# Kernel tuning notes

Measured on AMD Instinct MI355X. Metric: run time of the kernel, lower is better.

Reference implementation:

```python
import jax, jax.numpy as jnp
import numpy as np

B, S, D = 8, 1024, 512
H, DH, OUT = 8, 64, 512
EPS = 1e-6

def _ln(x, scale, bias):
    m = jnp.mean(x, -1, keepdims=True)
    v = jnp.mean(jnp.square(x - m), -1, keepdims=True)
    return (x - m) * jax.lax.rsqrt(v + EPS) * scale + bias

def _rel_shift(x):
    # TransformerXL relative shift: [B,H,Q,P] -> [B,H,Q,P]
    b, h, q, p = x.shape
    x = jnp.pad(x, ((0, 0), (0, 0), (0, 0), (1, 0)))
    x = x.reshape(b, h, p + 1, q)
    return x[:, :, 1:, :].reshape(b, h, q, p)

def _gate(x, y, wry, wrx, wzy, wzx, why, whx, bg):
    # GTrXL GRU-style gating
    r = jax.nn.sigmoid(y @ wry + x @ wrx)
    z = jax.nn.sigmoid(y @ wzy + x @ wzx - bg)
    h = jnp.tanh(y @ why + (r * x) @ whx)
    return (1 - z) * x + z * h

def setup_inputs() -> dict:
    key = jax.random.key(0)
    ks = jax.random.split(key, 40)
    w = lambda k, shp: (0.02 * jax.random.normal(k, shp, jnp.float32))
    inp = {
        'values_keys': jax.random.normal(ks[0], (B, S, D), jnp.float32),
        'queries': jax.random.normal(ks[1], (B, S, D), jnp.float32),
        'pos_embed': jax.random.normal(ks[2], (S, D), jnp.float32),
        'mask': jnp.tril(jnp.ones((S, S), bool))[None, None],
        'ln1_scale': jnp.ones((D,), jnp.float32), 'ln1_bias': jnp.zeros((D,), jnp.float32),
        'wq': w(ks[3], (D, H, DH)), 'bq': jnp.zeros((H, DH), jnp.float32),
        'wk': w(ks[4], (D, H, DH)), 'bk': jnp.zeros((H, DH), jnp.float32),
        'wv': w(ks[5], (D, H, DH)), 'bv': jnp.zeros((H, DH), jnp.float32),
        'wr': w(ks[6], (D, H, DH)),
        'u_bias': w(ks[7], (H, DH)), 'v_bias': w(ks[8], (H, DH)),
        'wo': w(ks[9], (H, DH, OUT)), 'bo': jnp.zeros((OUT,), jnp.float32),
        'ln2_scale': jnp.ones((OUT,), jnp.float32), 'ln2_bias': jnp.zeros((OUT,), jnp.float32),
        'w1': w(ks[10], (OUT, OUT)), 'b1': jnp.zeros((OUT,), jnp.float32),
        'w2': w(ks[11], (OUT, OUT)), 'b2': jnp.zeros((OUT,), jnp.float32),
    }
    for gi, base in ((1, 12), (2, 19)):
        for j, nm in enumerate(['wry', 'wrx', 'wzy', 'wzx', 'why', 'whx']):
            inp['g%d_%s' % (gi, nm)] = w(ks[base + j], (OUT, OUT))
        inp['g%d_bg' % gi] = 2.0 * jnp.ones((OUT,), jnp.float32)
    return inp

def reference(values_keys, queries, pos_embed, mask, ln1_scale, ln1_bias, wq, bq, wk, bk, wv, bv, wr, u_bias, v_bias, wo, bo, ln2_scale, ln2_bias, w1, b1, w2, b2, g1_wry, g1_wrx, g1_wzy, g1_wzx, g1_why, g1_whx, g1_bg, g2_wry, g2_wrx, g2_wzy, g2_wzx, g2_why, g2_whx, g2_bg):
    vk = _ln(values_keys, ln1_scale, ln1_bias)
    qn = _ln(queries, ln1_scale, ln1_bias)
    q = jnp.einsum('bsd,dhk->bshk', qn, wq) + bq
    k = jnp.einsum('bsd,dhk->bshk', vk, wk) + bk
    v = jnp.einsum('bsd,dhk->bshk', vk, wv) + bv
    r = jnp.einsum('pd,dhk->phk', pos_embed, wr)
    ac = jnp.einsum('bqhk,bshk->bhqs', q + u_bias, k)
    bd = _rel_shift(jnp.einsum('bqhk,phk->bhqp', q + v_bias, r))
    scores = (ac + bd) * jnp.float32(1.0 / np.sqrt(DH))
    scores = jnp.where(mask, scores, jnp.float32(-1e9))
    attn = jax.nn.softmax(scores, axis=-1)
    o = jnp.einsum('bhqs,bshk->bqhk', attn, v)
    attn_out = jnp.einsum('bqhk,hko->bqo', o, wo) + bo
    out_attention = _gate(queries, jax.nn.relu(attn_out), g1_wry, g1_wrx, g1_wzy, g1_wzx, g1_why, g1_whx, g1_bg)
    h = _ln(out_attention, ln2_scale, ln2_bias)
    h = jax.nn.gelu(h @ w1 + b1) @ w2 + b2
    return _gate(h, jax.nn.relu(out_attention), g2_wry, g2_wrx, g2_wzy, g2_wzx, g2_why, g2_whx, g2_bg)
```

## Files before the change

kernel.cpp:

```cpp
#include <hip/hip_runtime.h>
#include <hip/hip_bf16.h>
#include <math.h>

#define TPB 256
#define B_   8
#define S_   1024
#define D_   512
#define H_   8
#define DH_  64
#define MTOK (B_ * S_)
#define NEL  (MTOK * D_)
#define WMAT (D_ * D_)

typedef __attribute__((ext_vector_type(8))) short bf8;
typedef __attribute__((ext_vector_type(4))) float f4;

__device__ __forceinline__ float ld_any(const void* p, long i, bool bf) {
  if (bf) {
    unsigned u = (unsigned)((const unsigned short*)p)[i];
    union { unsigned u; float f; } c; c.u = u << 16;
    return c.f;
  }
  return ((const float*)p)[i];
}

__device__ __forceinline__ unsigned short f2bf(float f) {
  union { float f; unsigned u; } c; c.f = f;
  unsigned u = c.u;
  u += 0x7FFFu + ((u >> 16) & 1u);
  return (unsigned short)(u >> 16);
}

typedef const void __attribute__((address_space(1)))* gp_t;
typedef void __attribute__((address_space(3)))* lp_t;
__device__ __forceinline__ void gl16(const void* g, void* l) {
  __builtin_amdgcn_global_load_lds((gp_t)(uintptr_t)g,
                                   (lp_t)(unsigned)(uintptr_t)l, 16, 0, 0);
}

struct P19 { const void* p[19]; };
struct P14 { const void* p[14]; };

__device__ __forceinline__ void ln_row(const void* src, unsigned short* dst,
                                       long row, const void* scale,
                                       const void* bias, bool bf_s, bool bf_p,
                                       int t, float* red) {
  long base = row * 512;
  float a = ld_any(src, base + t, bf_s), b = ld_any(src, base + t + 256, bf_s);
  red[t] = a + b;
  __syncthreads();
  for (int s = 128; s > 0; s >>= 1) { if (t < s) red[t] += red[t + s]; __syncthreads(); }
  float m = red[0] * (1.0f / 512.0f);
  __syncthreads();
  float da = a - m, db = b - m;
  red[t] = da * da + db * db;
  __syncthreads();
  for (int s = 128; s > 0; s >>= 1) { if (t < s) red[t] += red[t + s]; __syncthreads(); }
  float inv = rsqrtf(red[0] * (1.0f / 512.0f) + 1e-6f);
  dst[base + t] = f2bf(da * inv * ld_any(scale, t, bf_p) + ld_any(bias, t, bf_p));
  dst[base + t + 256] =
      f2bf(db * inv * ld_any(scale, t + 256, bf_p) + ld_any(bias, t + 256, bf_p));
}

__global__ __launch_bounds__(TPB) void k_prep(
    const void* __restrict__ vk_src, const void* __restrict__ q_src,
    const void* __restrict__ pos_src, const void* __restrict__ sc_src,
    const void* __restrict__ bi_src, P19 pw, P14 pp,
    unsigned short* __restrict__ vk_b, unsigned short* __restrict__ qn_b,
    float* __restrict__ qF, unsigned short* __restrict__ qB,
    unsigned short* __restrict__ posB, float* __restrict__ Pb,
    unsigned short* __restrict__ Wt, const unsigned* __restrict__ flagp) {
  __shared__ float smem[64 * 65];
  const bool bf = (*flagp == 0x3F803F80u);
  const int bx = blockIdx.x, t = threadIdx.x;
  if (bx < 16384) {
    long row = bx;
    const void* src = vk_src; unsigned short* dst = vk_b;
    if (row >= MTOK) { src = q_src; dst = qn_b; row -= MTOK; }
    ln_row(src, dst, row, sc_src, bi_src, bf, bf, t, smem);
  } else if (bx < 34844) {
    int bid = bx - 16384;
    if (bid < 16384) {
      long i = (long)bid * TPB + t;
      float v = ld_any(q_src, i, bf);
      qF[i] = v; qB[i] = f2bf(v);
    } else if (bid < 18432) {
      long i = (long)(bid - 16384) * TPB + t;
      posB[i] = f2bf(ld_any(pos_src, i, bf));
    } else {
      int i = (bid - 18432) * TPB + t;
      Pb[i] = ld_any(pp.p[i >> 9], i & 511, bf);
    }
  } else {
    int zz = bx - 34844;
    int z = zz >> 6, tile = zz & 63;
    int k0 = (tile >> 3) * 64, n0 = (tile & 7) * 64;
    const void* src = pw.p[z];
    unsigned short* dst = Wt + (size_t)z * WMAT;
#pragma unroll
    for (int i = 0; i < 16; i++) {
      int fl = i * TPB + t;
      int r = fl >> 6, c = fl & 63;
      smem[r * 65 + c] = ld_any(src, (long)(k0 + r) * 512 + n0 + c, bf);
    }
    __syncthreads();
#pragma unroll
    for (int i = 0; i < 16; i++) {
      int fl = i * TPB + t;
      int r = fl >> 6, c = fl & 63;
      dst[(size_t)(n0 + r) * 512 + k0 + c] = f2bf(smem[c * 65 + r]);
    }
  }
}

__global__ __launch_bounds__(TPB) void k_ln_bf(const void* __restrict__ src,
                                               unsigned short* __restrict__ dst,
                                               const float* __restrict__ scale,
                                               const float* __restrict__ bias) {
  __shared__ float red[TPB];
  ln_row(src, dst, blockIdx.x, scale, bias, false, false, threadIdx.x, red);
}

__device__ __forceinline__ void gemm_core(
    unsigned short* As, unsigned short* Bs,
    const unsigned short* __restrict__ A1, const unsigned short* __restrict__ W1,
    const unsigned short* __restrict__ A2, const unsigned short* __restrict__ W2,
    const float* __restrict__ bias, const float* __restrict__ xb,
    const float* __restrict__ zb, const float* __restrict__ aux1,
    const float* __restrict__ aux2,
    float* __restrict__ outF, unsigned short* __restrict__ outB,
    unsigned short* __restrict__ outB2,
    const unsigned* __restrict__ flagp, int ACT, int bm, int bn) {
  const int tid = threadIdx.x;
  const int w = tid >> 6, lane = tid & 63;
  const int quad = lane >> 4, col = lane & 15;
  const int lrow = lane >> 3;
  const int lkc  = (lane & 7) ^ lrow;
  const int sw_base = col & 7;

  f4 acc[2][2];
#pragma unroll
  for (int mi = 0; mi < 2; mi++)
#pragma unroll
    for (int ni = 0; ni < 2; ni++) acc[mi][ni] = (f4){0.f, 0.f, 0.f, 0.f};

  for (int prod = 0; prod < 2; ++prod) {
    const unsigned short* Ap = prod ? A2 : A1;
    const unsigned short* Wp = prod ? W2 : W1;
    if (!Ap) break;
    for (int k0 = 0; k0 < 512; k0 += 64) {
      __syncthreads();
      gl16(Ap + (size_t)(bm + w * 8 + lrow) * 512 + k0 + lkc * 8,
           (char*)As + w * 1024);
      const unsigned short* bS = Wp + (size_t)(bn + w * 8 + lrow) * 512 + k0 + lkc * 8;
      gl16(bS,                    (char*)Bs + w * 1024);
      gl16(bS + (size_t)32 * 512, (char*)Bs + 4096 + w * 1024);
      gl16(bS + (size_t)64 * 512, (char*)Bs + 8192 + w * 1024);
      gl16(bS + (size_t)96 * 512, (char*)Bs + 12288 + w * 1024);
      __syncthreads();
#pragma unroll
      for (int kk = 0; kk < 2; ++kk) {
        const int swz = (kk * 4 + quad) ^ sw_base;
        bf8 af[2], bfg[2];
#pragma unroll
        for (int mi = 0; mi < 2; mi++)
          af[mi] = *(const bf8*)&As[((mi * 16 + col) * 8 + swz) * 8];
#pragma unroll
        for (int ni = 0; ni < 2; ni++)
          bfg[ni] = *(const bf8*)&Bs[((w * 32 + ni * 16 + col) * 8 + swz) * 8];
#pragma unroll
        for (int mi = 0; mi < 2; mi++)
#pragma unroll
          for (int ni = 0; ni < 2; ni++)
            acc[mi][ni] = __builtin_amdgcn_mfma_f32_16x16x32_bf16(af[mi], bfg[ni],
                                                                  acc[mi][ni], 0, 0, 0);
      }
    }
  }

  const bool bfout = flagp && (*flagp == 0x3F803F80u);
#pragma unroll
  for (int mi = 0; mi < 2; mi++)
#pragma unroll
    for (int ni = 0; ni < 2; ni++) {
      const int n = bn + w * 32 + ni * 16 + col;
      const float bn_v = bias ? bias[n] : 0.f;
      const int m0 = bm + mi * 16 + quad * 4;
      if (ACT == 11 && n >= 512) {
        unsigned long long pk = 0;
#pragma unroll
        for (int r = 0; r < 4; r++) {
          float v = acc[mi][ni][r] + bn_v;
          pk |= (unsigned long long)f2bf(v) << (16 * r);
        }
        size_t dst = ((size_t)(m0 >> 10) * 512 + (n - 512)) * 1024 + (m0 & 1023);
        *(unsigned long long*)&outB2[dst] = pk;
      } else {
#pragma unroll
        for (int r = 0; r < 4; r++) {
          size_t idx = (size_t)(m0 + r) * 512 + n;
          float v = acc[mi][ni][r] + bn_v;
          if (ACT == 0) {
            if (outF) outF[idx] = v;
            if (outB) outB[idx] = f2bf(v);
          } else if (ACT == 1) {
            outB[idx] = f2bf(fmaxf(v, 0.f));
          } else if (ACT == 5) {
            float z = zb[idx], x = xb[idx];
            float g = (1.f - z) * x + z * tanhf(v);
            outF[idx] = g;
            outB[idx] = f2bf(fmaxf(g, 0.f));
          } else if (ACT == 6) {
            float t = 0.7978845608028654f * (v + 0.044715f * v * v * v);
            outB[idx] = f2bf(0.5f * v * (1.f + tanhf(t)));
          } else if (ACT == 7) {
            float z = zb[idx], x = xb[idx];
            float g = (1.f - z) * x + z * tanhf(v);
            if (bfout) outB[idx] = f2bf(g);
            else       outF[idx] = g;
          } else if (ACT == 8) {
            outB[idx]  = f2bf(v + aux1[n]);
            outB2[idx] = f2bf(v + aux2[n]);
          } else if (ACT == 10) {
            if (n < 512) {
              outB[idx] = f2bf(xb[idx] / (1.f + __expf(-v)));
            } else {
              size_t zi = (size_t)(m0 + r) * 512 + (n - 512);
              outF[zi] = 1.f / (1.f + __expf(-(v - aux1[n - 512])));
            }
          } else if (ACT == 11) {
            outB[idx] = f2bf(v);
          }
        }
      }
    }
}

__global__ __launch_bounds__(TPB) void k_gemm(
    const unsigned short* __restrict__ A1, const unsigned short* __restrict__ W1,
    const unsigned short* __restrict__ A2, const unsigned short* __restrict__ W2,
    const float* __restrict__ bias, const float* __restrict__ xb,
    const float* __restrict__ zb, const float* __restrict__ aux1,
    const float* __restrict__ aux2,
    float* __restrict__ outF, unsigned short* __restrict__ outB,
    unsigned short* __restrict__ outB2,
    const unsigned* __restrict__ flagp, int ACT) {
  __shared__ unsigned short As[32 * 64];
  __shared__ unsigned short Bs[128 * 64];
  gemm_core(As, Bs, A1, W1, A2, W2, bias, xb, zb, aux1, aux2,
            outF, outB, outB2, flagp, ACT,
            blockIdx.x * 32, blockIdx.y * 128);
}

__global__ __launch_bounds__(TPB) void k_proj(
    const unsigned short* __restrict__ qn_b, const unsigned short* __restrict__ vk_b,
    const unsigned short* __restrict__ pos_b, const unsigned short* __restrict__ Wt,
    const float* __restrict__ Pb,
    unsigned short* __restrict__ qu_b, unsigned short* __restrict__ qv_b,
    unsigned short* __restrict__ k_b, unsigned short* __restrict__ vT,
    unsigned short* __restrict__ r_b) {
  __shared__ unsigned short As[32 * 64];
  __shared__ unsigned short Bs[128 * 64];
  const int bx = blockIdx.x;
  if (bx < 1024) {
    int bm = (bx & 255) * 32, bn = (bx >> 8) * 128;
    gemm_core(As, Bs, qn_b, Wt, nullptr, nullptr, Pb + 1024, nullptr, nullptr,
              Pb + 2560, Pb + 3072, nullptr, qu_b, qv_b, nullptr, 8, bm, bn);
  } else if (bx < 3072) {
    int t = bx - 1024;
    int bm = (t & 255) * 32, bn = (t >> 8) * 128;
    gemm_core(As, Bs, vk_b, Wt + (size_t)1 * WMAT, nullptr, nullptr, Pb + 1536,
              nullptr, nullptr, nullptr, nullptr, nullptr, k_b, vT, nullptr,
              11, bm, bn);
  } else {
    int t = bx - 3072;
    int bm = (t & 31) * 32, bn = (t >> 5) * 128;
    gemm_core(As, Bs, pos_b, Wt + (size_t)3 * WMAT, nullptr, nullptr, nullptr,
              nullptr, nullptr, nullptr, nullptr, nullptr, r_b, nullptr,
              nullptr, 0, bm, bn);
  }
}

#define AC_STR 68
#define BD_STR 100

__global__ __launch_bounds__(128) void k_attn3(
    const unsigned short* __restrict__ quB, const unsigned short* __restrict__ qvB,
    const unsigned short* __restrict__ kB, const unsigned short* __restrict__ vT,
    const unsigned short* __restrict__ rB, unsigned short* __restrict__ oB) {
  __shared__ float acS[2][16 * AC_STR];
  __shared__ float bdS[2][16 * BD_STR];
  const int tid = threadIdx.x;
  const int w = tid >> 6, lane = tid & 63;
  const int quad = lane >> 4, col = lane & 15;
  const int hh = w;
  const int bx = blockIdx.x;
  const int bh = (bx & 7) * 8 + ((bx >> 3) & 7);
  const int i  = bx >> 6;
  const int b = bh >> 3, h = bh & 7, dbase = h * 64;
  float* acw = acS[w];
  float* bdw = bdS[w];
  const float* acp = acS[w ^ 1];
  const float* bdp = bdS[w ^ 1];

  const int qts[2] = {63 - i, i};
#pragma unroll 1
  for (int ti = 0; ti < 2; ++ti) {
    const int qt = qts[ti];
    const int q0 = qt << 4;
    const int np = (qt >> 2) + 1;
    bf8 aqu[2], aqv[2];
    {
      const unsigned short* p1 = quB + (size_t)(b * 1024 + q0 + col) * 512 + dbase + quad * 8;
      const unsigned short* p2 = qvB + (size_t)(b * 1024 + q0 + col) * 512 + dbase + quad * 8;
      aqu[0] = *(const bf8*)p1; aqu[1] = *(const bf8*)(p1 + 32);
      aqv[0] = *(const bf8*)p2; aqv[1] = *(const bf8*)(p2 + 32);
    }
    f4 accO[4];
#pragma unroll
    for (int nd = 0; nd < 4; nd++) accO[nd] = (f4){0.f, 0.f, 0.f, 0.f};
    float lsum = 0.f;

#pragma unroll 1
    for (int pt = hh; pt < np; pt += 2) {
      const int p0 = pt << 6;
      const int j0 = 1008 - q0 + p0;
      f4 ac[4], bd[5];
#pragma unroll
      for (int ni = 0; ni < 4; ni++) ac[ni] = (f4){0.f, 0.f, 0.f, 0.f};
#pragma unroll
      for (int nj = 0; nj < 5; nj++) bd[nj] = (f4){0.f, 0.f, 0.f, 0.f};
#pragma unroll
      for (int ks = 0; ks < 2; ++ks) {
        const int dof = dbase + ks * 32 + quad * 8;
#pragma unroll
        for (int ni = 0; ni < 4; ++ni) {
          bf8 kb = *(const bf8*)&kB[(size_t)(b * 1024 + p0 + ni * 16 + col) * 512 + dof];
          ac[ni] = __builtin_amdgcn_mfma_f32_16x16x32_bf16(aqu[ks], kb, ac[ni], 0, 0, 0);
        }
#pragma unroll
        for (int nj = 0; nj < 5; ++nj) {
          int j = j0 + nj * 16 + col; if (j > 1023) j = 1023;
          bf8 rb = *(const bf8*)&rB[(size_t)j * 512 + dof];
          bd[nj] = __builtin_amdgcn_mfma_f32_16x16x32_bf16(aqv[ks], rb, bd[nj], 0, 0, 0);
        }
      }
#pragma unroll
      for (int ni = 0; ni < 4; ++ni)
#pragma unroll
        for (int r = 0; r < 4; ++r)
          acw[(quad * 4 + r) * AC_STR + ni * 16 + col] = ac[ni][r];
#pragma unroll
      for (int nj = 0; nj < 5; ++nj)
#pragma unroll
        for (int r = 0; r < 4; ++r) {
          int row = quad * 4 + r;
          bdw[row * BD_STR + 1 + nj * 16 + col + row] = bd[nj][r];
        }
      __asm__ volatile("s_waitcnt lgkmcnt(0)" ::: "memory");

      bf8 apf[2];
      const int qg = q0 + col;
#pragma unroll
      for (int ks = 0; ks < 2; ++ks) {
        const int po = ks * 32 + quad * 8;
        f4 A0 = *(const f4*)&acw[col * AC_STR + po];
        f4 A1 = *(const f4*)&acw[col * AC_STR + po + 4];
        f4 B0 = *(const f4*)&bdw[col * BD_STR + 16 + po];
        f4 B1 = *(const f4*)&bdw[col * BD_STR + 16 + po + 4];
        const int pb = p0 + po;
        union { bf8 v; unsigned short s[8]; } ap;
#pragma unroll
        for (int jj = 0; jj < 4; ++jj) {
          float e0 = (pb + jj <= qg) ? __expf((A0[jj] + B0[jj]) * 0.125f) : 0.f;
          float e1 = (pb + 4 + jj <= qg) ? __expf((A1[jj] + B1[jj]) * 0.125f) : 0.f;
          lsum += e0 + e1;
          ap.s[jj] = f2bf(e0); ap.s[4 + jj] = f2bf(e1);
        }
        apf[ks] = ap.v;
      }
#pragma unroll
      for (int ks = 0; ks < 2; ++ks) {
#pragma unroll
        for (int nd = 0; nd < 4; ++nd) {
          bf8 vb = *(const bf8*)&vT[(size_t)(bh * 64 + nd * 16 + col) * 1024 +
                                    p0 + ks * 32 + quad * 8];
          accO[nd] = __builtin_amdgcn_mfma_f32_16x16x32_bf16(apf[ks], vb, accO[nd], 0, 0, 0);
        }
      }
    }

#pragma unroll
    for (int nd = 0; nd < 4; ++nd)
#pragma unroll
      for (int r = 0; r < 4; ++r)
        acw[lane * 17 + nd * 4 + r] = accO[nd][r];
    bdw[lane] = lsum;
    __syncthreads();
    if (hh == 0) {
#pragma unroll
      for (int nd = 0; nd < 4; ++nd)
#pragma unroll
        for (int r = 0; r < 4; ++r)
          accO[nd][r] += acp[lane * 17 + nd * 4 + r];
      float ls = lsum + bdp[lane];
      ls += __shfl_xor(ls, 16, 64);
      ls += __shfl_xor(ls, 32, 64);
      float lr[4];
#pragma unroll
      for (int r = 0; r < 4; ++r) lr[r] = __shfl(ls, quad * 4 + r, 64);
#pragma unroll
      for (int nd = 0; nd < 4; ++nd)
#pragma unroll
        for (int r = 0; r < 4; ++r) {
          float o = accO[nd][r] / lr[r];
          oB[(size_t)(b * 1024 + q0 + quad * 4 + r) * 512 + dbase + nd * 16 + col] = f2bf(o);
        }
    }
    __syncthreads();
  }
}

extern "C" void kernel_launch(void* const* d_in, const int* in_sizes, int n_in,
                              void* d_out, int out_size, void* d_ws, size_t ws_size,
                              hipStream_t stream) {
  (void)in_sizes; (void)n_in; (void)out_size; (void)ws_size;
  const unsigned* flagp = (const unsigned*)d_in[4];
  char* ws = (char*)d_ws;
  const size_t MB = 1u << 20;
  auto SH = [&](int i) { return (unsigned short*)(ws + (size_t)i * 8 * MB); };

  unsigned short* vk_b = SH(0);
  unsigned short* qn_b = SH(1);
  unsigned short* qu_b = SH(2);
  unsigned short* qv_b = SH(3);
  unsigned short* k_b  = SH(4);
  unsigned short* qr_b = SH(5);
  unsigned short* vT   = SH(6);
  unsigned short* posr = SH(7);
  float* qF = (float*)(ws + 64 * MB);
  float* z1 = (float*)(ws + 80 * MB);
  float* oa = (float*)(ws + 96 * MB);
  unsigned short* Wt = (unsigned short*)(ws + 112 * MB);
  float* Pb = (float*)(ws + 122 * MB);

  unsigned short* pos_b = posr;
  unsigned short* r_b   = posr + 524288;
  unsigned short* o_b = qn_b;  unsigned short* y1 = vk_b;
  unsigned short* rx1 = qu_b;  unsigned short* y2 = qv_b;
  unsigned short* ln2h = k_b;  unsigned short* hg = qr_b;
  unsigned short* h_b = vT;    unsigned short* rx2 = posr;
  float* hF = qF;              float* z2 = z1;

  auto W = [&](int i) { return Wt + (size_t)i * WMAT; };
  dim3 bt(TPB);
  dim3 gG(MTOK / 32, 4);
  dim3 gG2(MTOK / 32, 8);

  P19 pw; const int wi[19] = {6, 8, 10, 12, 15, 19, 21,
                              23, 25, 24, 26, 27, 28, 30, 32, 31, 33, 34, 35};
  for (int i = 0; i < 19; i++) pw.p[i] = d_in[wi[i]];
  P14 pp; const int pi[14] = {4, 5, 7, 9, 11, 13, 14, 16, 17, 18, 20, 22, 29, 36};
  for (int i = 0; i < 14; i++) pp.p[i] = d_in[pi[i]];

  k_prep<<<dim3(36060), bt, 0, stream>>>(d_in[0], d_in[1], d_in[2], d_in[4],
                                         d_in[5], pw, pp, vk_b, qn_b, qF, qr_b,
                                         pos_b, Pb, Wt, flagp);

  k_proj<<<dim3(3200), bt, 0, stream>>>(qn_b, vk_b, pos_b, Wt, Pb,
                                        qu_b, qv_b, k_b, vT, r_b);

  k_attn3<<<dim3(2048), dim3(128), 0, stream>>>(qu_b, qv_b, k_b, vT, r_b, o_b);

  k_gemm<<<gG, bt, 0, stream>>>(o_b, W(4), nullptr, nullptr, Pb + 3584, nullptr,
                                nullptr, nullptr, nullptr, nullptr, y1, nullptr,
                                nullptr, 1);
  k_gemm<<<gG2, bt, 0, stream>>>(y1, W(7), qr_b, W(9), nullptr, qF, nullptr,
                                 Pb + 6144, nullptr, z1, rx1, nullptr,
                                 nullptr, 10);
  k_gemm<<<gG, bt, 0, stream>>>(y1, W(11), rx1, W(12), nullptr, qF, z1,
                                nullptr, nullptr, oa, y2, nullptr, nullptr, 5);

  k_ln_bf<<<dim3(MTOK), bt, 0, stream>>>(oa, ln2h, Pb + 4096, Pb + 4608);
  k_gemm<<<gG, bt, 0, stream>>>(ln2h, W(5), nullptr, nullptr, Pb + 5120, nullptr,
                                nullptr, nullptr, nullptr, nullptr, hg, nullptr,
                                nullptr, 6);
  k_gemm<<<gG, bt, 0, stream>>>(hg, W(6), nullptr, nullptr, Pb + 5632, nullptr,
                                nullptr, nullptr, nullptr, hF, h_b, nullptr,
                                nullptr, 0);

  k_gemm<<<gG2, bt, 0, stream>>>(y2, W(13), h_b, W(15), nullptr, hF, nullptr,
                                 Pb + 6656, nullptr, z2, rx2, nullptr,
                                 nullptr, 10);
  k_gemm<<<gG, bt, 0, stream>>>(y2, W(17), rx2, W(18), nullptr, hF, z2,
                                nullptr, nullptr, (float*)d_out,
                                (unsigned short*)d_out, nullptr, flagp, 7);
}
```

Measured before the change: 541.0 us.

## Use one wave per query tile in attention, dropping intra-block split and reduction

The attention kernel now launches 4096 single-wave blocks, each owning one 16-row query tile and walking all of its key tiles. Previously each 2-wave block handled a paired short and long query tile for load balance and split key tiles across waves, merging partial sums through shared memory with barriers. The new layout removes the cross-wave merge and syncs and shrinks the bd shared buffer with a bounds-checked shifted write. In exchange, blocks now vary widely in work (causal tiles from 1 to 16 key tiles), so load balance depends on the scheduler, and each wave's loop is serial.

```diff
diff --git a/kernel.cpp b/kernel.cpp
--- a/kernel.cpp
+++ b/kernel.cpp
@@ -282,143 +282,118 @@
 }
 
 #define AC_STR 68
-#define BD_STR 100
-
-__global__ __launch_bounds__(128) void k_attn3(
+#define BD_STR 68
+
+__global__ __launch_bounds__(64, 4) void k_attn4(
     const unsigned short* __restrict__ quB, const unsigned short* __restrict__ qvB,
     const unsigned short* __restrict__ kB, const unsigned short* __restrict__ vT,
     const unsigned short* __restrict__ rB, unsigned short* __restrict__ oB) {
-  __shared__ float acS[2][16 * AC_STR];
-  __shared__ float bdS[2][16 * BD_STR];
-  const int tid = threadIdx.x;
-  const int w = tid >> 6, lane = tid & 63;
+  __shared__ float acS[16 * AC_STR];
+  __shared__ float bdS[16 * BD_STR];
+  const int lane = threadIdx.x;
   const int quad = lane >> 4, col = lane & 15;
-  const int hh = w;
   const int bx = blockIdx.x;
   const int bh = (bx & 7) * 8 + ((bx >> 3) & 7);
-  const int i  = bx >> 6;
+  const int qt = 63 - (bx >> 6);
   const int b = bh >> 3, h = bh & 7, dbase = h * 64;
-  float* acw = acS[w];
-  float* bdw = bdS[w];
-  const float* acp = acS[w ^ 1];
-  const float* bdp = bdS[w ^ 1];
-
-  const int qts[2] = {63 - i, i};
+  const int q0 = qt << 4;
+  const int np = (qt >> 2) + 1;
+
+  bf8 aqu[2], aqv[2];
+  {
+    const unsigned short* p1 = quB + (size_t)(b * 1024 + q0 + col) * 512 + dbase + quad * 8;
+    const unsigned short* p2 = qvB + (size_t)(b * 1024 + q0 + col) * 512 + dbase + quad * 8;
+    aqu[0] = *(const bf8*)p1; aqu[1] = *(const bf8*)(p1 + 32);
+    aqv[0] = *(const bf8*)p2; aqv[1] = *(const bf8*)(p2 + 32);
+  }
+  f4 accO[4];
+#pragma unroll
+  for (int nd = 0; nd < 4; nd++) accO[nd] = (f4){0.f, 0.f, 0.f, 0.f};
+  float lsum = 0.f;
+
 #pragma unroll 1
-  for (int ti = 0; ti < 2; ++ti) {
-    const int qt = qts[ti];
-    const int q0 = qt << 4;
-    const int np = (qt >> 2) + 1;
-    bf8 aqu[2], aqv[2];
-    {
-      const unsigned short* p1 = quB + (size_t)(b * 1024 + q0 + col) * 512 + dbase + quad * 8;
-      const unsigned short* p2 = qvB + (size_t)(b * 1024 + q0 + col) * 512 + dbase + quad * 8;
-      aqu[0] = *(const bf8*)p1; aqu[1] = *(const bf8*)(p1 + 32);
-      aqv[0] = *(const bf8*)p2; aqv[1] = *(const bf8*)(p2 + 32);
-    }
-    f4 accO[4];
-#pragma unroll
-    for (int nd = 0; nd < 4; nd++) accO[nd] = (f4){0.f, 0.f, 0.f, 0.f};
-    float lsum = 0.f;
-
-#pragma unroll 1
-    for (int pt = hh; pt < np; pt += 2) {
-      const int p0 = pt << 6;
-      const int j0 = 1008 - q0 + p0;
-      f4 ac[4], bd[5];
-#pragma unroll
-      for (int ni = 0; ni < 4; ni++) ac[ni] = (f4){0.f, 0.f, 0.f, 0.f};
-#pragma unroll
-      for (int nj = 0; nj < 5; nj++) bd[nj] = (f4){0.f, 0.f, 0.f, 0.f};
-#pragma unroll
-      for (int ks = 0; ks < 2; ++ks) {
-        const int dof = dbase + ks * 32 + quad * 8;
-#pragma unroll
-        for (int ni = 0; ni < 4; ++ni) {
-          bf8 kb = *(const bf8*)&kB[(size_t)(b * 1024 + p0 + ni * 16 + col) * 512 + dof];
-          ac[ni] = __builtin_amdgcn_mfma_f32_16x16x32_bf16(aqu[ks], kb, ac[ni], 0, 0, 0);
-        }
-#pragma unroll
-        for (int nj = 0; nj < 5; ++nj) {
-          int j = j0 + nj * 16 + col; if (j > 1023) j = 1023;
-          bf8 rb = *(const bf8*)&rB[(size_t)j * 512 + dof];
-          bd[nj] = __builtin_amdgcn_mfma_f32_16x16x32_bf16(aqv[ks], rb, bd[nj], 0, 0, 0);
-        }
-      }
-#pragma unroll
-      for (int ni = 0; ni < 4; ++ni)
-#pragma unroll
-        for (int r = 0; r < 4; ++r)
-          acw[(quad * 4 + r) * AC_STR + ni * 16 + col] = ac[ni][r];
-#pragma unroll
-      for (int nj = 0; nj < 5; ++nj)
-#pragma unroll
-        for (int r = 0; r < 4; ++r) {
-          int row = quad * 4 + r;
-          bdw[row * BD_STR + 1 + nj * 16 + col + row] = bd[nj][r];
-        }
-      __asm__ volatile("s_waitcnt lgkmcnt(0)" ::: "memory");
-
-      bf8 apf[2];
-      const int qg = q0 + col;
-#pragma unroll
-      for (int ks = 0; ks < 2; ++ks) {
-        const int po = ks * 32 + quad * 8;
-        f4 A0 = *(const f4*)&acw[col * AC_STR + po];
-        f4 A1 = *(const f4*)&acw[col * AC_STR + po + 4];
-        f4 B0 = *(const f4*)&bdw[col * BD_STR + 16 + po];
-        f4 B1 = *(const f4*)&bdw[col * BD_STR + 16 + po + 4];
-        const int pb = p0 + po;
-        union { bf8 v; unsigned short s[8]; } ap;
-#pragma unroll
-        for (int jj = 0; jj < 4; ++jj) {
-          float e0 = (pb + jj <= qg) ? __expf((A0[jj] + B0[jj]) * 0.125f) : 0.f;
-          float e1 = (pb + 4 + jj <= qg) ? __expf((A1[jj] + B1[jj]) * 0.125f) : 0.f;
-          lsum += e0 + e1;
-          ap.s[jj] = f2bf(e0); ap.s[4 + jj] = f2bf(e1);
-        }
-        apf[ks] = ap.v;
-      }
-#pragma unroll
-      for (int ks = 0; ks < 2; ++ks) {
-#pragma unroll
-        for (int nd = 0; nd < 4; ++nd) {
-          bf8 vb = *(const bf8*)&vT[(size_t)(bh * 64 + nd * 16 + col) * 1024 +
-                                    p0 + ks * 32 + quad * 8];
-          accO[nd] = __builtin_amdgcn_mfma_f32_16x16x32_bf16(apf[ks], vb, accO[nd], 0, 0, 0);
-        }
-      }
-    }
-
-#pragma unroll
-    for (int nd = 0; nd < 4; ++nd)
+  for (int pt = 0; pt < np; ++pt) {
+    const int p0 = pt << 6;
+    const int j0 = 1008 - q0 + p0;
+    f4 ac[4], bd[5];
+#pragma unroll
+    for (int ni = 0; ni < 4; ni++) ac[ni] = (f4){0.f, 0.f, 0.f, 0.f};
+#pragma unroll
+    for (int nj = 0; nj < 5; nj++) bd[nj] = (f4){0.f, 0.f, 0.f, 0.f};
+#pragma unroll
+    for (int ks = 0; ks < 2; ++ks) {
+      const int dof = dbase + ks * 32 + quad * 8;
+#pragma unroll
+      for (int ni = 0; ni < 4; ++ni) {
+        bf8 kb = *(const bf8*)&kB[(size_t)(b * 1024 + p0 + ni * 16 + col) * 512 + dof];
+        ac[ni] = __builtin_amdgcn_mfma_f32_16x16x32_bf16(aqu[ks], kb, ac[ni], 0, 0, 0);
+      }
+#pragma unroll
+      for (int nj = 0; nj < 5; ++nj) {
+        int j = j0 + nj * 16 + col; if (j > 1023) j = 1023;
+        bf8 rb = *(const bf8*)&rB[(size_t)j * 512 + dof];
+        bd[nj] = __builtin_amdgcn_mfma_f32_16x16x32_bf16(aqv[ks], rb, bd[nj], 0, 0, 0);
+      }
+    }
+#pragma unroll
+    for (int ni = 0; ni < 4; ++ni)
 #pragma unroll
       for (int r = 0; r < 4; ++r)
-        acw[lane * 17 + nd * 4 + r] = accO[nd][r];
-    bdw[lane] = lsum;
-    __syncthreads();
-    if (hh == 0) {
-#pragma unroll
-      for (int nd = 0; nd < 4; ++nd)
-#pragma unroll
-        for (int r = 0; r < 4; ++r)
-          accO[nd][r] += acp[lane * 17 + nd * 4 + r];
-      float ls = lsum + bdp[lane];
-      ls += __shfl_xor(ls, 16, 64);
-      ls += __shfl_xor(ls, 32, 64);
-      float lr[4];
-#pragma unroll
-      for (int r = 0; r < 4; ++r) lr[r] = __shfl(ls, quad * 4 + r, 64);
-#pragma unroll
-      for (int nd = 0; nd < 4; ++nd)
-#pragma unroll
-        for (int r = 0; r < 4; ++r) {
-          float o = accO[nd][r] / lr[r];
-          oB[(size_t)(b * 1024 + q0 + quad * 4 + r) * 512 + dbase + nd * 16 + col] = f2bf(o);
-        }
-    }
-    __syncthreads();
-  }
+        acS[(quad * 4 + r) * AC_STR + ni * 16 + col] = ac[ni][r];
+#pragma unroll
+    for (int nj = 0; nj < 5; ++nj)
+#pragma unroll
+      for (int r = 0; r < 4; ++r) {
+        int row = quad * 4 + r;
+        int idx = nj * 16 + col + row - 15;
+        if ((unsigned)idx < 64u) bdS[row * BD_STR + idx] = bd[nj][r];
+      }
+    __asm__ volatile("s_waitcnt lgkmcnt(0)" ::: "memory");
+
+    bf8 apf[2];
+    const int qg = q0 + col;
+#pragma unroll
+    for (int ks = 0; ks < 2; ++ks) {
+      const int po = ks * 32 + quad * 8;
+      f4 A0 = *(const f4*)&acS[col * AC_STR + po];
+      f4 A1 = *(const f4*)&acS[col * AC_STR + po + 4];
+      f4 B0 = *(const f4*)&bdS[col * BD_STR + po];
+      f4 B1 = *(const f4*)&bdS[col * BD_STR + po + 4];
+      const int pb = p0 + po;
+      union { bf8 v; unsigned short s[8]; } ap;
+#pragma unroll
+      for (int jj = 0; jj < 4; ++jj) {
+        float e0 = (pb + jj <= qg) ? __expf((A0[jj] + B0[jj]) * 0.125f) : 0.f;
+        float e1 = (pb + 4 + jj <= qg) ? __expf((A1[jj] + B1[jj]) * 0.125f) : 0.f;
+        lsum += e0 + e1;
+        ap.s[jj] = f2bf(e0); ap.s[4 + jj] = f2bf(e1);
+      }
+      apf[ks] = ap.v;
+    }
+#pragma unroll
+    for (int ks = 0; ks < 2; ++ks) {
+#pragma unroll
+      for (int nd = 0; nd < 4; ++nd) {
+        bf8 vb = *(const bf8*)&vT[(size_t)(bh * 64 + nd * 16 + col) * 1024 +
+                                  p0 + ks * 32 + quad * 8];
+        accO[nd] = __builtin_amdgcn_mfma_f32_16x16x32_bf16(apf[ks], vb, accO[nd], 0, 0, 0);
+      }
+    }
+  }
+
+  float ls = lsum;
+  ls += __shfl_xor(ls, 16, 64);
+  ls += __shfl_xor(ls, 32, 64);
+  float lr[4];
+#pragma unroll
+  for (int r = 0; r < 4; ++r) lr[r] = __shfl(ls, quad * 4 + r, 64);
+#pragma unroll
+  for (int nd = 0; nd < 4; ++nd)
+#pragma unroll
+    for (int r = 0; r < 4; ++r) {
+      float o = accO[nd][r] / lr[r];
+      oB[(size_t)(b * 1024 + q0 + quad * 4 + r) * 512 + dbase + nd * 16 + col] = f2bf(o);
+    }
 }
 
 extern "C" void kernel_launch(void* const* d_in, const int* in_sizes, int n_in,
@@ -470,7 +445,7 @@
   k_proj<<<dim3(3200), bt, 0, stream>>>(qn_b, vk_b, pos_b, Wt, Pb,
                                         qu_b, qv_b, k_b, vT, r_b);
 
-  k_attn3<<<dim3(2048), dim3(128), 0, stream>>>(qu_b, qv_b, k_b, vT, r_b, o_b);
+  k_attn4<<<dim3(4096), dim3(64), 0, stream>>>(qu_b, qv_b, k_b, vT, r_b, o_b);
 
   k_gemm<<<gG, bt, 0, stream>>>(o_b, W(4), nullptr, nullptr, Pb + 3584, nullptr,
                                 nullptr, nullptr, nullptr, nullptr, y1, nullptr,
```

New measurement: 517.4 us. 4.4% less time.
